# Optimization experiments

Hardware: AMD Instinct MI355X
Metric: run time of the kernel (lower is better)

Reference implementation:

```python
import jax, jax.numpy as jnp
import numpy as np

EPS = 1e-12  # torch F.normalize eps
SIGMA_RBF = 1.0  # rbf bandwidth (init arg sigma=1)


def _l2norm(v, axis=-1):
    return v / jnp.maximum(jnp.linalg.norm(v, axis=axis, keepdims=True), EPS)


def setup_inputs() -> dict:
    key = jax.random.key(0)
    kx, kw, kb, ku, kc = jax.random.split(key, 5)
    B, C, E, F = 512, 100, 2048, 128
    x = jax.random.normal(kx, (B, E), dtype=jnp.float32)
    # per-class Linear weights [C, F, E] and biases [C, F] (torch Linear layout: out x in)
    bound = 1.0 / np.sqrt(E)
    W = jax.random.uniform(kw, (C, F, E), minval=-bound, maxval=bound, dtype=jnp.float32)
    b = jax.random.uniform(kb, (C, F), minval=-bound, maxval=bound, dtype=jnp.float32)
    # spectral-norm power-iteration vectors u (one per class, normalized)
    u = _l2norm(jax.random.normal(ku, (C, F), dtype=jnp.float32))
    # centroid buffer c (EMA means; randn stand-in for a trained state)
    c = jax.random.normal(kc, (C, F), dtype=jnp.float32)
    return {"x": x, "W": W, "b": b, "u": u, "c": c}


def reference(x, W, b, u, c):
    # --- spectral norm: one power-iteration step per class (torch default) ---
    v = _l2norm(jnp.einsum('cfe,cf->ce', W, u))        # v = normalize(W^T u)  [C,E]
    u2 = _l2norm(jnp.einsum('cfe,ce->cf', W, v))       # u = normalize(W v)    [C,F]
    sigma = jnp.einsum('cf,cfe,ce->c', u2, W, v)       # sigma = u^T W v       [C]
    Wn = W / sigma[:, None, None]
    # --- fused per-class linear projections: z[b,c,f] ---
    z = jnp.einsum('be,cfe->bcf', x, Wn) + b[None, :, :]
    # --- RBF to centroids: exp(-||c - z||^2 / (2 sigma^2)) ---
    dist2 = jnp.sum((c[None, :, :] - z) ** 2, axis=-1)  # [B, C]
    probs = jnp.exp(-dist2 / (2.0 * SIGMA_RBF ** 2))
    return probs
```

## Files before the change

### kernel.cpp

```cpp
#include <hip/hip_runtime.h>
#include <math.h>

#define B_ 512
#define C_ 100
#define E_ 2048
#define F_ 128
#define NCHUNK 16
#define CHUNKW 128

typedef _Float16 f16x8 __attribute__((ext_vector_type(8)));
typedef float    f32x4 __attribute__((ext_vector_type(4)));

#define AS1q __attribute__((address_space(1)))
#define AS3q __attribute__((address_space(3)))

__device__ __forceinline__ void gl_lds16(const void* g, void* lds_base) {
    __builtin_amdgcn_global_load_lds((const AS1q void*)g, (AS3q void*)lds_base, 16, 0, 0);
}

__device__ __forceinline__ f16x8 frag_ld(const float* T, int r, int p) {
    const int k = r & 15;
    const int b = r << 6;
    const f32x4 lo = *(const f32x4*)&T[b + ((((p << 1))     ^ k) << 2)];
    const f32x4 hi = *(const f32x4*)&T[b + ((((p << 1) | 1) ^ k) << 2)];
    f16x8 fr;
    fr[0] = (_Float16)lo[0]; fr[1] = (_Float16)lo[1];
    fr[2] = (_Float16)lo[2]; fr[3] = (_Float16)lo[3];
    fr[4] = (_Float16)hi[0]; fr[5] = (_Float16)hi[1];
    fr[6] = (_Float16)hi[2]; fr[7] = (_Float16)hi[3];
    return fr;
}

__global__ __launch_bounds__(256, 3)
void k_gram(const float* __restrict__ W, _Float16* __restrict__ Wh,
            const float* __restrict__ x, _Float16* __restrict__ xh,
            const float* __restrict__ u, float* __restrict__ ychunks) {
    const int b = blockIdx.x;
    const int t = threadIdx.x;

    if (b >= 1600) {
        const size_t base = (size_t)(b - 1600) * 32768 + t * 8;
#pragma unroll
        for (int it = 0; it < 16; ++it) {
            const size_t idx = base + (size_t)it * 2048;
            float4 a  = *(const float4*)(x + idx);
            float4 bb = *(const float4*)(x + idx + 4);
            f16x8 h;
            h[0] = (_Float16)a.x;  h[1] = (_Float16)a.y;  h[2] = (_Float16)a.z;  h[3] = (_Float16)a.w;
            h[4] = (_Float16)bb.x; h[5] = (_Float16)bb.y; h[6] = (_Float16)bb.z; h[7] = (_Float16)bb.w;
            *(f16x8*)(xh + idx) = h;
        }
        return;
    }

    const int c     = b >> 4;
    const int chunk = b & 15;
    const int w  = t >> 6;
    const int l  = t & 63;
    const int wm = w & 1, wn = w >> 1;
    const int ln = l & 15, quad = l >> 4;

    __shared__ float Ts[128 * 64];

    f32x4 acc[4][4];
#pragma unroll
    for (int mt = 0; mt < 4; ++mt)
#pragma unroll
        for (int nt = 0; nt < 4; ++nt) acc[mt][nt] = (f32x4){0.f, 0.f, 0.f, 0.f};

    const int lrow4 = l >> 4, cs = l & 15;
    const float* wbase = W + (size_t)c * F_ * E_ + chunk * CHUNKW;

    const int cr = t >> 1, cb = (t & 1) * 32;
    _Float16* wdst = Wh + ((size_t)c * F_ + cr) * E_ + chunk * CHUNKW + cb;

#pragma unroll
    for (int it = 0; it < CHUNKW / 64; ++it) {
        const int k0 = it * 64;
#pragma unroll
        for (int qq = 0; qq < 8; ++qq) {
            const int q   = w * 8 + qq;
            const int r   = q * 4 + lrow4;
            const int off = ((cs ^ (r & 15)) << 2);
            gl_lds16(wbase + (size_t)r * E_ + k0 + off, &Ts[q * 256]);
        }
        __syncthreads();

        {
            f32x4 v[8];
#pragma unroll
            for (int j = 0; j < 8; ++j) {
                const int g = (cb >> 2) + j;
                v[j] = *(const f32x4*)&Ts[cr * 64 + ((g ^ (cr & 15)) << 2)];
            }
#pragma unroll
            for (int j = 0; j < 4; ++j) {
                f16x8 h;
                h[0] = (_Float16)v[2*j][0]; h[1] = (_Float16)v[2*j][1];
                h[2] = (_Float16)v[2*j][2]; h[3] = (_Float16)v[2*j][3];
                h[4] = (_Float16)v[2*j+1][0]; h[5] = (_Float16)v[2*j+1][1];
                h[6] = (_Float16)v[2*j+1][2]; h[7] = (_Float16)v[2*j+1][3];
                *(f16x8*)(wdst + k0 + j * 8) = h;
            }
        }

#pragma unroll
        for (int kk = 0; kk < 64; kk += 32) {
            const int pb = quad + (kk >> 3);
            f16x8 av[4], bv[4];
#pragma unroll
            for (int mt = 0; mt < 4; ++mt)
                av[mt] = frag_ld(Ts, wm * 64 + mt * 16 + ln, pb);
#pragma unroll
            for (int nt = 0; nt < 4; ++nt)
                bv[nt] = frag_ld(Ts, wn * 64 + nt * 16 + ln, pb);
#pragma unroll
            for (int mt = 0; mt < 4; ++mt)
#pragma unroll
                for (int nt = 0; nt < 4; ++nt)
                    acc[mt][nt] = __builtin_amdgcn_mfma_f32_16x16x32_f16(
                        av[mt], bv[nt], acc[mt][nt], 0, 0, 0);
        }
        __syncthreads();
    }

    const float* uc = u + (size_t)c * F_;
    float un[4];
#pragma unroll
    for (int nt = 0; nt < 4; ++nt) un[nt] = uc[wn * 64 + nt * 16 + ln];

    float* red = (float*)&Ts[0];

#pragma unroll
    for (int mt = 0; mt < 4; ++mt) {
#pragma unroll
        for (int rr = 0; rr < 4; ++rr) {
            float py = acc[mt][0][rr] * un[0];
            py = fmaf(acc[mt][1][rr], un[1], py);
            py = fmaf(acc[mt][2][rr], un[2], py);
            py = fmaf(acc[mt][3][rr], un[3], py);
            py += __shfl_xor(py, 1, 64);
            py += __shfl_xor(py, 2, 64);
            py += __shfl_xor(py, 4, 64);
            py += __shfl_xor(py, 8, 64);
            if (ln == 0) {
                int m = wm * 64 + mt * 16 + quad * 4 + rr;
                red[m * 2 + wn] = py;
            }
        }
    }
    __syncthreads();
    if (t < 128) {
        float yv = red[t * 2] + red[t * 2 + 1];
        ychunks[((size_t)chunk * C_ + c) * F_ + t] = yv;
    }
}

__global__ __launch_bounds__(256, 3)
void k_main(const _Float16* __restrict__ xh, const _Float16* __restrict__ Wh,
            const float* __restrict__ bias, const float* __restrict__ cent,
            const float* __restrict__ u, const float* __restrict__ ychunks,
            float* __restrict__ out) {
    const int c  = blockIdx.y;
    const int b0 = blockIdx.x * 128;
    const int t  = threadIdx.x;
    const int w  = t >> 6;
    const int l  = t & 63;
    const int wm = w & 1, wn = w >> 1;
    const int ln = l & 15, quad = l >> 4;

    __shared__ _Float16 Xs[128 * 64];
    __shared__ _Float16 Ws[128 * 64];
    __shared__ float red2[2][2];
    __shared__ float s_rsig;

    if (t < 128) {
        float yf = 0.f;
#pragma unroll
        for (int ch = 0; ch < NCHUNK; ++ch)
            yf += ychunks[((size_t)ch * C_ + c) * F_ + t];
        float nvp = u[(size_t)c * F_ + t] * yf;
        float tsp = yf * yf;
        for (int off = 32; off; off >>= 1) {
            nvp += __shfl_down(nvp, off, 64);
            tsp += __shfl_down(tsp, off, 64);
        }
        if (l == 0) { red2[w][0] = nvp; red2[w][1] = tsp; }
    }
    __syncthreads();
    if (t == 0) s_rsig = sqrtf((red2[0][0] + red2[1][0]) / (red2[0][1] + red2[1][1]));

    f32x4 acc[4][4];
#pragma unroll
    for (int mt = 0; mt < 4; ++mt)
#pragma unroll
        for (int nt = 0; nt < 4; ++nt) acc[mt][nt] = (f32x4){0.f, 0.f, 0.f, 0.f};

    const int lr = l >> 3;
    const int lg = (l & 7) ^ lr;
    const _Float16* xsrc = xh + (size_t)(b0 + w * 32 + lr) * E_ + lg * 8;
    const _Float16* wsrc = Wh + ((size_t)c * F_ + w * 32 + lr) * E_ + lg * 8;

    for (int k0 = 0; k0 < E_; k0 += 64) {
#pragma unroll
        for (int q = 0; q < 4; ++q)
            gl_lds16(xsrc + (size_t)q * 8 * E_ + k0, &Xs[(w * 4 + q) * 512]);
#pragma unroll
        for (int q = 0; q < 4; ++q)
            gl_lds16(wsrc + (size_t)q * 8 * E_ + k0, &Ws[(w * 4 + q) * 512]);
        __syncthreads();

#pragma unroll
        for (int kk = 0; kk < 64; kk += 32) {
            const int g0 = (kk >> 3) + quad;
            const int sw = (g0 ^ (ln & 7)) * 8;
            f16x8 av[4], bv[4];
#pragma unroll
            for (int mt = 0; mt < 4; ++mt)
                av[mt] = *(const f16x8*)&Xs[(wm * 64 + mt * 16 + ln) * 64 + sw];
#pragma unroll
            for (int nt = 0; nt < 4; ++nt)
                bv[nt] = *(const f16x8*)&Ws[(wn * 64 + nt * 16 + ln) * 64 + sw];
#pragma unroll
            for (int mt = 0; mt < 4; ++mt)
#pragma unroll
                for (int nt = 0; nt < 4; ++nt)
                    acc[mt][nt] = __builtin_amdgcn_mfma_f32_16x16x32_f16(
                        av[mt], bv[nt], acc[mt][nt], 0, 0, 0);
        }
        __syncthreads();
    }

    const float rsigma = s_rsig;

    float bi[4], ce[4];
#pragma unroll
    for (int nt = 0; nt < 4; ++nt) {
        int f = wn * 64 + nt * 16 + ln;
        bi[nt] = bias[c * F_ + f];
        ce[nt] = cent[c * F_ + f];
    }

    float* red = (float*)&Xs[0];

#pragma unroll
    for (int mt = 0; mt < 4; ++mt) {
#pragma unroll
        for (int r = 0; r < 4; ++r) {
            float part = 0.f;
#pragma unroll
            for (int nt = 0; nt < 4; ++nt) {
                float z = fmaf(acc[mt][nt][r], rsigma, bi[nt]);
                float d = ce[nt] - z;
                part = fmaf(d, d, part);
            }
            part += __shfl_xor(part, 1, 64);
            part += __shfl_xor(part, 2, 64);
            part += __shfl_xor(part, 4, 64);
            part += __shfl_xor(part, 8, 64);
            if (ln == 0) {
                int m = wm * 64 + mt * 16 + quad * 4 + r;
                red[m * 2 + wn] = part;
            }
        }
    }
    __syncthreads();
    if (t < 128) {
        float d2 = red[t * 2] + red[t * 2 + 1];
        out[(size_t)(b0 + t) * C_ + c] = expf(-0.5f * d2);
    }
}

extern "C" void kernel_launch(void* const* d_in, const int* in_sizes, int n_in,
                              void* d_out, int out_size, void* d_ws, size_t ws_size,
                              hipStream_t stream) {
    const float* x  = (const float*)d_in[0];
    const float* W  = (const float*)d_in[1];
    const float* b  = (const float*)d_in[2];
    const float* u  = (const float*)d_in[3];
    const float* cc = (const float*)d_in[4];
    float* out = (float*)d_out;

    char* ws = (char*)d_ws;
    _Float16* Wh      = (_Float16*)ws;
    _Float16* xh      = (_Float16*)(ws + (size_t)C_ * F_ * E_ * 2);
    float*    ychunks = (float*)(ws + (size_t)C_ * F_ * E_ * 2 + (size_t)B_ * E_ * 2);

    k_gram<<<1632, 256, 0, stream>>>(W, Wh, x, xh, u, ychunks);

    dim3 grid(B_ / 128, C_);
    k_main<<<grid, 256, 0, stream>>>(xh, Wh, b, cc, u, ychunks, out);
}
```

Before: 216.0 us.

## Replace per-chunk Gram MFMA with two matrix-vector products for power iteration

The spectral-norm pre-pass no longer builds a 128x128 Gram matrix per class chunk with f16 MFMA and then multiplies it by u. It computes v_chunk = W_chunk^T u and then y = W_chunk v_chunk as two fp32 matrix-vector products from the same LDS tile. This relies on associativity and cuts the per-chunk compute from cubic to quadratic in the tile size. It also keeps fp32 precision, adds an extra barrier and small LDS buffers, and raises the occupancy hint in launch bounds from 3 to 4.

After: 216.4 us. Within noise of the previous version (+0.2%).

```diff
diff --git a/kernel.cpp b/kernel.cpp
--- a/kernel.cpp
+++ b/kernel.cpp
@@ -18,20 +18,7 @@
     __builtin_amdgcn_global_load_lds((const AS1q void*)g, (AS3q void*)lds_base, 16, 0, 0);
 }
 
-__device__ __forceinline__ f16x8 frag_ld(const float* T, int r, int p) {
-    const int k = r & 15;
-    const int b = r << 6;
-    const f32x4 lo = *(const f32x4*)&T[b + ((((p << 1))     ^ k) << 2)];
-    const f32x4 hi = *(const f32x4*)&T[b + ((((p << 1) | 1) ^ k) << 2)];
-    f16x8 fr;
-    fr[0] = (_Float16)lo[0]; fr[1] = (_Float16)lo[1];
-    fr[2] = (_Float16)lo[2]; fr[3] = (_Float16)lo[3];
-    fr[4] = (_Float16)hi[0]; fr[5] = (_Float16)hi[1];
-    fr[6] = (_Float16)hi[2]; fr[7] = (_Float16)hi[3];
-    return fr;
-}
-
-__global__ __launch_bounds__(256, 3)
+__global__ __launch_bounds__(256, 4)
 void k_gram(const float* __restrict__ W, _Float16* __restrict__ Wh,
             const float* __restrict__ x, _Float16* __restrict__ xh,
             const float* __restrict__ u, float* __restrict__ ychunks) {
@@ -55,24 +42,27 @@
 
     const int c     = b >> 4;
     const int chunk = b & 15;
-    const int w  = t >> 6;
-    const int l  = t & 63;
-    const int wm = w & 1, wn = w >> 1;
-    const int ln = l & 15, quad = l >> 4;
+    const int w = t >> 6;
+    const int l = t & 63;
+    const int lrow4 = l >> 4, cs = l & 15;
 
     __shared__ float Ts[128 * 64];
-
-    f32x4 acc[4][4];
-#pragma unroll
-    for (int mt = 0; mt < 4; ++mt)
-#pragma unroll
-        for (int nt = 0; nt < 4; ++nt) acc[mt][nt] = (f32x4){0.f, 0.f, 0.f, 0.f};
-
-    const int lrow4 = l >> 4, cs = l & 15;
+    __shared__ float vs[64];
+    __shared__ float us[128];
+    __shared__ float yred[256];
+
     const float* wbase = W + (size_t)c * F_ * E_ + chunk * CHUNKW;
 
     const int cr = t >> 1, cb = (t & 1) * 32;
     _Float16* wdst = Wh + ((size_t)c * F_ + cr) * E_ + chunk * CHUNKW + cb;
+
+    if (t < 128) us[t] = u[(size_t)c * F_ + t];
+
+    const int ae = t >> 2;
+    const int af = (t & 3) * 32;
+    const int gch = ae >> 2, el = ae & 3;
+
+    float yacc = 0.f;
 
 #pragma unroll
     for (int it = 0; it < CHUNKW / 64; ++it) {
@@ -87,73 +77,48 @@
         __syncthreads();
 
         {
-            f32x4 v[8];
-#pragma unroll
-            for (int j = 0; j < 8; ++j) {
-                const int g = (cb >> 2) + j;
-                v[j] = *(const f32x4*)&Ts[cr * 64 + ((g ^ (cr & 15)) << 2)];
+            float p = 0.f;
+#pragma unroll
+            for (int j = 0; j < 32; ++j) {
+                const int f = af + j;
+                p = fmaf(Ts[(f << 6) + (((gch ^ (f & 15)) << 2) | el)], us[f], p);
             }
-#pragma unroll
-            for (int j = 0; j < 4; ++j) {
-                f16x8 h;
-                h[0] = (_Float16)v[2*j][0]; h[1] = (_Float16)v[2*j][1];
-                h[2] = (_Float16)v[2*j][2]; h[3] = (_Float16)v[2*j][3];
-                h[4] = (_Float16)v[2*j+1][0]; h[5] = (_Float16)v[2*j+1][1];
-                h[6] = (_Float16)v[2*j+1][2]; h[7] = (_Float16)v[2*j+1][3];
-                *(f16x8*)(wdst + k0 + j * 8) = h;
-            }
-        }
-
-#pragma unroll
-        for (int kk = 0; kk < 64; kk += 32) {
-            const int pb = quad + (kk >> 3);
-            f16x8 av[4], bv[4];
-#pragma unroll
-            for (int mt = 0; mt < 4; ++mt)
-                av[mt] = frag_ld(Ts, wm * 64 + mt * 16 + ln, pb);
-#pragma unroll
-            for (int nt = 0; nt < 4; ++nt)
-                bv[nt] = frag_ld(Ts, wn * 64 + nt * 16 + ln, pb);
-#pragma unroll
-            for (int mt = 0; mt < 4; ++mt)
-#pragma unroll
-                for (int nt = 0; nt < 4; ++nt)
-                    acc[mt][nt] = __builtin_amdgcn_mfma_f32_16x16x32_f16(
-                        av[mt], bv[nt], acc[mt][nt], 0, 0, 0);
-        }
-        __syncthreads();
-    }
-
-    const float* uc = u + (size_t)c * F_;
-    float un[4];
-#pragma unroll
-    for (int nt = 0; nt < 4; ++nt) un[nt] = uc[wn * 64 + nt * 16 + ln];
-
-    float* red = (float*)&Ts[0];
-
-#pragma unroll
-    for (int mt = 0; mt < 4; ++mt) {
-#pragma unroll
-        for (int rr = 0; rr < 4; ++rr) {
-            float py = acc[mt][0][rr] * un[0];
-            py = fmaf(acc[mt][1][rr], un[1], py);
-            py = fmaf(acc[mt][2][rr], un[2], py);
-            py = fmaf(acc[mt][3][rr], un[3], py);
-            py += __shfl_xor(py, 1, 64);
-            py += __shfl_xor(py, 2, 64);
-            py += __shfl_xor(py, 4, 64);
-            py += __shfl_xor(py, 8, 64);
-            if (ln == 0) {
-                int m = wm * 64 + mt * 16 + quad * 4 + rr;
-                red[m * 2 + wn] = py;
-            }
-        }
-    }
+            p += __shfl_xor(p, 1, 64);
+            p += __shfl_xor(p, 2, 64);
+            if ((t & 3) == 0) vs[ae] = p;
+        }
+
+        f32x4 cv[8];
+#pragma unroll
+        for (int j = 0; j < 8; ++j) {
+            const int g = (cb >> 2) + j;
+            cv[j] = *(const f32x4*)&Ts[cr * 64 + ((g ^ (cr & 15)) << 2)];
+        }
+#pragma unroll
+        for (int j = 0; j < 4; ++j) {
+            f16x8 h;
+            h[0] = (_Float16)cv[2*j][0];   h[1] = (_Float16)cv[2*j][1];
+            h[2] = (_Float16)cv[2*j][2];   h[3] = (_Float16)cv[2*j][3];
+            h[4] = (_Float16)cv[2*j+1][0]; h[5] = (_Float16)cv[2*j+1][1];
+            h[6] = (_Float16)cv[2*j+1][2]; h[7] = (_Float16)cv[2*j+1][3];
+            *(f16x8*)(wdst + k0 + j * 8) = h;
+        }
+        __syncthreads();
+
+#pragma unroll
+        for (int j = 0; j < 8; ++j) {
+            const f32x4 vv = *(const f32x4*)&vs[cb + j * 4];
+            yacc = fmaf(cv[j][0], vv[0], yacc);
+            yacc = fmaf(cv[j][1], vv[1], yacc);
+            yacc = fmaf(cv[j][2], vv[2], yacc);
+            yacc = fmaf(cv[j][3], vv[3], yacc);
+        }
+    }
+
+    yred[cr * 2 + (t & 1)] = yacc;
     __syncthreads();
-    if (t < 128) {
-        float yv = red[t * 2] + red[t * 2 + 1];
-        ychunks[((size_t)chunk * C_ + c) * F_ + t] = yv;
-    }
+    if (t < 128)
+        ychunks[((size_t)chunk * C_ + c) * F_ + t] = yred[t * 2] + yred[t * 2 + 1];
 }
 
 __global__ __launch_bounds__(256, 3)
```
